# Kernel optimization log

Hardware: AMD Instinct MI355X
Metric: run time of the kernel (lower is better)

## Reference

```python
import jax, jax.numpy as jnp
import numpy as np

BATCH, N_FEATURES, D_MODEL = 8192, 8192, 1024


def setup_inputs() -> dict:
    key = jax.random.key(0)
    kx, kw = jax.random.split(key)
    # x: sparse feature activations in the original (COO); dense uniform here.
    x = jax.random.uniform(kx, (BATCH, N_FEATURES), dtype=jnp.float32)
    # Xavier-normal init for W_tr [n_features, d_model].
    std = float(np.sqrt(2.0 / (N_FEATURES + D_MODEL)))
    W_tr = jax.random.normal(kw, (N_FEATURES, D_MODEL), dtype=jnp.float32) * std
    bias = jnp.zeros((N_FEATURES,), dtype=jnp.float32)
    return {"x": x, "W_tr": W_tr, "bias": bias}


def reference(x, W_tr, bias):
    # h = x @ W_tr              : [B, n_features] @ [n_features, d_model] -> [B, d_model]
    # out = relu(h @ W_tr.T + b): [B, d_model] @ [d_model, n_features] -> [B, n_features]
    h = jnp.einsum("bf,fd->bd", x, W_tr)
    return jax.nn.relu(jnp.einsum("bd,fd->bf", h, W_tr) + bias)
```

## Files before the change

### kernel.cpp

```cpp
#include <hip/hip_runtime.h>
#include <hip/hip_bf16.h>
#include <stdint.h>

#define BATCH  8192
#define NFEAT  8192
#define DMODEL 1024

typedef unsigned short u16;
typedef __attribute__((ext_vector_type(8))) short  short8;
typedef __attribute__((ext_vector_type(4))) float  f32x4;

__device__ __forceinline__ u16 f2b(float f) {
    uint32_t u = __float_as_uint(f);
    u += 0x7fffu + ((u >> 16) & 1u);
    return (u16)(u >> 16);
}

__device__ __forceinline__ void gld16(const u16* g, void* l) {
    __builtin_amdgcn_global_load_lds(
        (const __attribute__((address_space(1))) void*)(uintptr_t)g,
        (__attribute__((address_space(3))) void*)(uint32_t)(uintptr_t)l,
        16, 0, 0);
}


__global__ void cvt_x_kernel(const float* __restrict__ x, u16* __restrict__ xb) {
    int i = blockIdx.x * blockDim.x + threadIdx.x;
    const float4* xv = (const float4*)x;
    float4 a = xv[2 * i];
    float4 b = xv[2 * i + 1];
    union { u16 u[8]; uint4 v; } o;
    o.u[0] = f2b(a.x); o.u[1] = f2b(a.y); o.u[2] = f2b(a.z); o.u[3] = f2b(a.w);
    o.u[4] = f2b(b.x); o.u[5] = f2b(b.y); o.u[6] = f2b(b.z); o.u[7] = f2b(b.w);
    ((uint4*)xb)[i] = o.v;
}

__global__ void cvt_w_kernel(const float* __restrict__ W,
                             u16* __restrict__ wb, u16* __restrict__ wt) {
    __shared__ u16 tile[64][65];
    const int f0 = blockIdx.x * 64;
    const int d0 = blockIdx.y * 64;
    const int t  = threadIdx.x;
#pragma unroll
    for (int rep = 0; rep < 16; ++rep) {
        int idx = rep * 256 + t;
        int r = idx >> 6, c = idx & 63;
        float v = W[(size_t)(f0 + r) * DMODEL + d0 + c];
        u16 u = f2b(v);
        tile[r][c] = u;
        wb[(size_t)(f0 + r) * DMODEL + d0 + c] = u;
    }
    __syncthreads();
#pragma unroll
    for (int rep = 0; rep < 16; ++rep) {
        int idx = rep * 256 + t;
        int r = idx >> 6, c = idx & 63;
        wt[(size_t)(d0 + r) * NFEAT + f0 + c] = tile[c][r];
    }
}

#define CBAR() do { asm volatile("" ::: "memory"); __builtin_amdgcn_s_barrier(); } while (0)


__global__ __launch_bounds__(512, 2)
void gemm1_relax(const u16* __restrict__ A, const u16* __restrict__ B,
                 u16* __restrict__ H, int N, int K) {
    const int NT = K >> 6;
    __shared__ __align__(1024) char lds[131072];
    const int BOFF = 98304;

    const int tid  = threadIdx.x;
    const int lane = tid & 63;
    const int wave = tid >> 6;
    const int wm   = wave >> 2;
    const int wn   = wave & 3;

    const int nwg = gridDim.x;
    const int swz = (blockIdx.x & 7) * (nwg >> 3) + (blockIdx.x >> 3);
    const int ntn = N >> 7;
    const int tm0 = (swz / ntn) << 8;
    const int tn0 = (swz % ntn) << 7;

    const int sr8 = lane >> 3;
    const int sg  = (lane & 7) ^ sr8;
    const int l15 = lane & 15, lhi = lane >> 4;
    const int ch0 = ((lhi ^ (lane & 7)) << 4);

    auto STAGE_A = [&](int tau) {
        if (tau < NT) {
            char* d = lds + (tau % 3) * 32768 + wave * 4096;
#pragma unroll
            for (int i = 0; i < 4; ++i)
                gld16(A + (size_t)(tm0 + wave * 32 + i * 8 + sr8) * K + ((size_t)tau << 6) + sg * 8,
                      d + i * 1024);
        }
    };
    auto STAGE_B = [&](int tau) {
        if (tau < NT) {
            char* d = lds + BOFF + (tau & 1) * 16384 + wave * 2048;
#pragma unroll
            for (int i = 0; i < 2; ++i)
                gld16(B + (size_t)(tn0 + wave * 16 + i * 8 + sr8) * K + ((size_t)tau << 6) + sg * 8,
                      d + i * 1024);
        }
    };

    short8 a0[4][2], a1[4][2];
    short8 b[2][2];
    f32x4  acc[8][2] = {};

    const char* Ab;
    const char* Bb;
    auto LDA0 = [&] {
#pragma unroll
        for (int fm = 0; fm < 4; ++fm) {
            a0[fm][0] = *(const short8*)(Ab + fm * 2048 + ch0);
            a0[fm][1] = *(const short8*)(Ab + fm * 2048 + (ch0 ^ 64));
        }
    };
    auto LDA1 = [&] {
#pragma unroll
        for (int fm = 0; fm < 4; ++fm) {
            a1[fm][0] = *(const short8*)(Ab + (4 + fm) * 2048 + ch0);
            a1[fm][1] = *(const short8*)(Ab + (4 + fm) * 2048 + (ch0 ^ 64));
        }
    };
    auto LDB_ = [&](int nh) {
        b[nh][0] = *(const short8*)(Bb + nh * 2048 + ch0);
        b[nh][1] = *(const short8*)(Bb + nh * 2048 + (ch0 ^ 64));
    };
    auto MMA0 = [&](int nh) {
#pragma unroll
        for (int ks = 0; ks < 2; ++ks)
#pragma unroll
            for (int fm = 0; fm < 4; ++fm)
                acc[fm][nh] = __builtin_amdgcn_mfma_f32_16x16x32_bf16(
                    a0[fm][ks], b[nh][ks], acc[fm][nh], 0, 0, 0);
    };
    auto MMA1 = [&](int nh) {
#pragma unroll
        for (int ks = 0; ks < 2; ++ks)
#pragma unroll
            for (int fm = 0; fm < 4; ++fm)
                acc[4 + fm][nh] = __builtin_amdgcn_mfma_f32_16x16x32_bf16(
                    a1[fm][ks], b[nh][ks], acc[4 + fm][nh], 0, 0, 0);
    };

    STAGE_A(0); STAGE_B(0);
    STAGE_A(1); STAGE_B(1);
    asm volatile("s_waitcnt vmcnt(6)" ::: "memory");
    __builtin_amdgcn_s_barrier();

    for (int t = 0; t < NT; ++t) {
        Ab = lds + (t % 3) * 32768 + wm * 16384 + l15 * 128;
        Bb = lds + BOFF + (t & 1) * 16384 + wn * 4096 + l15 * 128;

        LDB_(0); LDB_(1); LDA0(); LDA1();
        STAGE_A(t + 2);
        __builtin_amdgcn_s_setprio(1);
        MMA0(0); MMA0(1);
        __builtin_amdgcn_s_setprio(0);
        CBAR();
        STAGE_B(t + 2);
        __builtin_amdgcn_s_setprio(1);
        MMA1(1); MMA1(0);
        __builtin_amdgcn_s_setprio(0);
        if (t < NT - 2)       asm volatile("s_waitcnt vmcnt(6)" ::: "memory");
        else if (t == NT - 2) asm volatile("s_waitcnt vmcnt(0)" ::: "memory");
        CBAR();
    }

    u16* lu = (u16*)lds;
#pragma unroll
    for (int fm = 0; fm < 8; ++fm)
#pragma unroll
        for (int nh = 0; nh < 2; ++nh) {
            const int col  = wn * 32 + nh * 16 + l15;
            const int row0 = wm * 128 + fm * 16 + lhi * 4;
#pragma unroll
            for (int r = 0; r < 4; ++r)
                lu[(row0 + r) * 128 + col] = f2b(acc[fm][nh][r]);
        }
    __syncthreads();
    const uint4* ls = (const uint4*)lds;
#pragma unroll
    for (int s = 0; s < 8; ++s) {
        int i = s * 512 + tid;
        int row = i >> 4;
        int col = (i & 15) * 8;
        *(uint4*)(H + (size_t)(tm0 + row) * N + (tn0 + col)) = ls[i];
    }
}

__global__ __launch_bounds__(512, 2)
void gemm2_persist(const u16* __restrict__ A, const u16* __restrict__ B,
                   float* __restrict__ O, const float* __restrict__ bias,
                   int N, int K) {
    __shared__ __align__(1024) char lds[163840];
    const int BOFF = 98304;
    const int TTOT = 64;

    const int tid  = threadIdx.x;
    const int lane = tid & 63;
    const int wave = tid >> 6;
    const int wm   = wave >> 2;
    const int wn   = wave & 3;

    const int bid = blockIdx.x;
    const int xcd = bid & 7;
    const int sub = (bid >> 3) & 3;
    const int mg  = bid >> 5;
    const int tn0     = ((xcd << 2) + sub) << 8;
    const int tm_base = mg << 10;

    const int sr8 = lane >> 3;
    const int sg  = (lane & 7) ^ sr8;
    const int l15 = lane & 15, lhi = lane >> 4;
    const int ch0 = ((lhi ^ (lane & 7)) << 4);

    auto STAGE_A = [&](int tau) {
        if (tau < TTOT) {
            char* d = lds + (tau % 3) * 32768 + wave * 4096;
            const int rb = tm_base + ((tau >> 4) << 8) + wave * 32 + sr8;
            const size_t co = ((size_t)(tau & 15) << 6) + sg * 8;
#pragma unroll
            for (int i = 0; i < 4; ++i)
                gld16(A + (size_t)(rb + i * 8) * K + co, d + i * 1024);
        }
    };
    auto STAGE_B = [&](int tau) {
        if (tau < TTOT) {
            char* d = lds + BOFF + (tau & 1) * 32768 + wave * 4096;
            const int rb = tn0 + wave * 32 + sr8;
            const size_t co = ((size_t)(tau & 15) << 6) + sg * 8;
#pragma unroll
            for (int i = 0; i < 4; ++i)
                gld16(B + (size_t)(rb + i * 8) * K + co, d + i * 1024);
        }
    };

    short8 a0[4][2], a1[4][2];
    short8 b[4][2];
    f32x4  acc[8][4] = {};

    const char* Ab;
    const char* Bb;
    auto LDA0 = [&] {
#pragma unroll
        for (int fm = 0; fm < 4; ++fm) {
            a0[fm][0] = *(const short8*)(Ab + fm * 2048 + ch0);
            a0[fm][1] = *(const short8*)(Ab + fm * 2048 + (ch0 ^ 64));
        }
    };
    auto LDA1 = [&] {
#pragma unroll
        for (int fm = 0; fm < 4; ++fm) {
            a1[fm][0] = *(const short8*)(Ab + (4 + fm) * 2048 + ch0);
            a1[fm][1] = *(const short8*)(Ab + (4 + fm) * 2048 + (ch0 ^ 64));
        }
    };
    auto LDB_ = [&](int nh) {
#pragma unroll
        for (int fn = 0; fn < 2; ++fn) {
            b[nh * 2 + fn][0] = *(const short8*)(Bb + (nh * 2 + fn) * 2048 + ch0);
            b[nh * 2 + fn][1] = *(const short8*)(Bb + (nh * 2 + fn) * 2048 + (ch0 ^ 64));
        }
    };
    auto MMA0 = [&](int nh) {
#pragma unroll
        for (int ks = 0; ks < 2; ++ks)
#pragma unroll
            for (int fm = 0; fm < 4; ++fm)
#pragma unroll
                for (int fn = 0; fn < 2; ++fn)
                    acc[fm][nh * 2 + fn] = __builtin_amdgcn_mfma_f32_16x16x32_bf16(
                        a0[fm][ks], b[nh * 2 + fn][ks], acc[fm][nh * 2 + fn], 0, 0, 0);
    };
    auto MMA1 = [&](int nh) {
#pragma unroll
        for (int ks = 0; ks < 2; ++ks)
#pragma unroll
            for (int fm = 0; fm < 4; ++fm)
#pragma unroll
                for (int fn = 0; fn < 2; ++fn)
                    acc[4 + fm][nh * 2 + fn] = __builtin_amdgcn_mfma_f32_16x16x32_bf16(
                        a1[fm][ks], b[nh * 2 + fn][ks], acc[4 + fm][nh * 2 + fn], 0, 0, 0);
    };

    const int ocol = tn0 + wn * 64;
    float bv[4];
#pragma unroll
    for (int fn = 0; fn < 4; ++fn) bv[fn] = bias[ocol + fn * 16 + l15];

    STAGE_A(0); STAGE_B(0);
    STAGE_A(1); STAGE_B(1);
    asm volatile("s_waitcnt vmcnt(8)" ::: "memory");
    __builtin_amdgcn_s_barrier();

    for (int tt = 0; tt < TTOT; ++tt) {
        Ab = lds + (tt % 3) * 32768 + wm * 16384 + l15 * 128;
        Bb = lds + BOFF + (tt & 1) * 32768 + wn * 8192 + l15 * 128;

        LDB_(0); LDB_(1); LDA0(); LDA1();
        STAGE_A(tt + 2);
        __builtin_amdgcn_s_setprio(1);
        MMA0(0); MMA0(1);
        __builtin_amdgcn_s_setprio(0);
        CBAR();
        STAGE_B(tt + 2);
        __builtin_amdgcn_s_setprio(1);
        MMA1(1); MMA1(0);
        __builtin_amdgcn_s_setprio(0);
        if (tt < TTOT - 2)       asm volatile("s_waitcnt vmcnt(8)" ::: "memory");
        else if (tt == TTOT - 2) asm volatile("s_waitcnt vmcnt(0)" ::: "memory");
        CBAR();

        if ((tt & 15) == 15) {
            const int orow = tm_base + ((tt >> 4) << 8) + wm * 128;
#pragma unroll
            for (int fm = 0; fm < 8; ++fm) {
                const int row0 = orow + fm * 16 + lhi * 4;
#pragma unroll
                for (int fn = 0; fn < 4; ++fn) {
                    const int col = ocol + fn * 16 + l15;
#pragma unroll
                    for (int r = 0; r < 4; ++r) {
                        float v = acc[fm][fn][r] + bv[fn];
                        O[(size_t)(row0 + r) * N + col] = v > 0.f ? v : 0.f;
                        acc[fm][fn][r] = 0.f;
                    }
                }
            }
        }
    }
}


extern "C" void kernel_launch(void* const* d_in, const int* in_sizes, int n_in,
                              void* d_out, int out_size, void* d_ws, size_t ws_size,
                              hipStream_t stream) {
    const float* x    = (const float*)d_in[0];
    const float* W    = (const float*)d_in[1];
    const float* bias = (const float*)d_in[2];
    float* out = (float*)d_out;

    char* ws = (char*)d_ws;
    u16* xb = (u16*)ws;
    u16* wt = (u16*)(ws + 134217728);
    u16* wb = (u16*)(ws + 134217728 + 16777216);
    u16* hb = (u16*)(ws + 134217728 + 2 * 16777216);

    cvt_x_kernel<<<(BATCH * NFEAT / 8) / 256, 256, 0, stream>>>(x, xb);
    cvt_w_kernel<<<dim3(NFEAT / 64, DMODEL / 64), 256, 0, stream>>>(W, wb, wt);

    gemm1_relax<<<dim3((BATCH / 256) * (DMODEL / 128)), 512, 0, stream>>>(
        xb, wt, hb, DMODEL, NFEAT);

    gemm2_persist<<<dim3(256), 512, 0, stream>>>(
        hb, wb, out, bias, NFEAT, DMODEL);
}
```

Before: 367.2 us.

## Restructure both GEMMs into finer-grained ping-pong pipeline with per-quarter staging

Both GEMM kernels drop the triple-buffered A tile and use double buffering, which cuts LDS use (gemm1 from 128KB to 96KB, gemm2 from 160KB to 128KB). Each K-step is split into four MFMA phases, each bracketed by barriers. Global-to-LDS loads for A and B are issued in quarter/half chunks interleaved between phases, so load issue is spread across the compute instead of bunched. The tradeoffs are many more barriers per iteration and a shallower prefetch depth, which could stall if memory latency is not hidden.

```diff
diff --git a/kernel.cpp b/kernel.cpp
--- a/kernel.cpp
+++ b/kernel.cpp
@@ -59,15 +59,18 @@
     }
 }
 
-#define CBAR() do { asm volatile("" ::: "memory"); __builtin_amdgcn_s_barrier(); } while (0)
+#define SYNC_IN()  do { __builtin_amdgcn_s_barrier(); \
+                        asm volatile("s_waitcnt lgkmcnt(0)" ::: "memory"); } while (0)
+#define SYNC_OUT() do { __builtin_amdgcn_s_setprio(0); __builtin_amdgcn_s_barrier(); } while (0)
 
 
 __global__ __launch_bounds__(512, 2)
-void gemm1_relax(const u16* __restrict__ A, const u16* __restrict__ B,
-                 u16* __restrict__ H, int N, int K) {
+void gemm1_m201(const u16* __restrict__ A, const u16* __restrict__ B,
+                u16* __restrict__ H, int N, int K) {
     const int NT = K >> 6;
-    __shared__ __align__(1024) char lds[131072];
-    const int BOFF = 98304;
+    const int NIT = NT >> 1;
+    __shared__ __align__(1024) char lds[98304];
+    const int BOFF = 65536;
 
     const int tid  = threadIdx.x;
     const int lane = tid & 63;
@@ -86,22 +89,20 @@
     const int l15 = lane & 15, lhi = lane >> 4;
     const int ch0 = ((lhi ^ (lane & 7)) << 4);
 
-    auto STAGE_A = [&](int tau) {
+    auto STA = [&](int tau, int q) {
         if (tau < NT) {
-            char* d = lds + (tau % 3) * 32768 + wave * 4096;
-#pragma unroll
-            for (int i = 0; i < 4; ++i)
-                gld16(A + (size_t)(tm0 + wave * 32 + i * 8 + sr8) * K + ((size_t)tau << 6) + sg * 8,
-                      d + i * 1024);
-        }
-    };
-    auto STAGE_B = [&](int tau) {
+            const size_t co = ((size_t)tau << 6) + sg * 8;
+#pragma unroll
+            for (int j = 0; j < 2; ++j)
+                gld16(A + (size_t)(tm0 + j * 128 + q * 64 + wave * 8 + sr8) * K + co,
+                      lds + (tau & 1) * 32768 + q * 16384 + j * 8192 + wave * 1024);
+        }
+    };
+    auto STB = [&](int tau, int nh) {
         if (tau < NT) {
-            char* d = lds + BOFF + (tau & 1) * 16384 + wave * 2048;
-#pragma unroll
-            for (int i = 0; i < 2; ++i)
-                gld16(B + (size_t)(tn0 + wave * 16 + i * 8 + sr8) * K + ((size_t)tau << 6) + sg * 8,
-                      d + i * 1024);
+            const size_t co = ((size_t)tau << 6) + sg * 8;
+            gld16(B + (size_t)(tn0 + (wave >> 1) * 32 + nh * 16 + (wave & 1) * 8 + sr8) * K + co,
+                  lds + BOFF + (tau & 1) * 16384 + nh * 8192 + (wave >> 1) * 2048 + (wave & 1) * 1024);
         }
     };
 
@@ -109,25 +110,26 @@
     short8 b[2][2];
     f32x4  acc[8][2] = {};
 
-    const char* Ab;
-    const char* Bb;
-    auto LDA0 = [&] {
+    auto LDA0 = [&](int p) {
+        const char* Ab = lds + p * 32768 + wm * 8192 + l15 * 128;
 #pragma unroll
         for (int fm = 0; fm < 4; ++fm) {
             a0[fm][0] = *(const short8*)(Ab + fm * 2048 + ch0);
             a0[fm][1] = *(const short8*)(Ab + fm * 2048 + (ch0 ^ 64));
         }
     };
-    auto LDA1 = [&] {
+    auto LDA1 = [&](int p) {
+        const char* Ab = lds + p * 32768 + 16384 + wm * 8192 + l15 * 128;
 #pragma unroll
         for (int fm = 0; fm < 4; ++fm) {
-            a1[fm][0] = *(const short8*)(Ab + (4 + fm) * 2048 + ch0);
-            a1[fm][1] = *(const short8*)(Ab + (4 + fm) * 2048 + (ch0 ^ 64));
-        }
-    };
-    auto LDB_ = [&](int nh) {
-        b[nh][0] = *(const short8*)(Bb + nh * 2048 + ch0);
-        b[nh][1] = *(const short8*)(Bb + nh * 2048 + (ch0 ^ 64));
+            a1[fm][0] = *(const short8*)(Ab + fm * 2048 + ch0);
+            a1[fm][1] = *(const short8*)(Ab + fm * 2048 + (ch0 ^ 64));
+        }
+    };
+    auto LDB_ = [&](int p, int nh) {
+        const char* Bb = lds + BOFF + p * 16384 + nh * 8192 + wn * 2048 + l15 * 128;
+        b[nh][0] = *(const short8*)(Bb + ch0);
+        b[nh][1] = *(const short8*)(Bb + (ch0 ^ 64));
     };
     auto MMA0 = [&](int nh) {
 #pragma unroll
@@ -146,28 +148,68 @@
                     a1[fm][ks], b[nh][ks], acc[4 + fm][nh], 0, 0, 0);
     };
 
-    STAGE_A(0); STAGE_B(0);
-    STAGE_A(1); STAGE_B(1);
-    asm volatile("s_waitcnt vmcnt(6)" ::: "memory");
+    STA(0, 0); STB(0, 0); STA(0, 1); STB(0, 1);
+    STA(1, 0); STB(1, 0); STA(1, 1);
+    asm volatile("s_waitcnt vmcnt(5)" ::: "memory");
     __builtin_amdgcn_s_barrier();
 
-    for (int t = 0; t < NT; ++t) {
-        Ab = lds + (t % 3) * 32768 + wm * 16384 + l15 * 128;
-        Bb = lds + BOFF + (t & 1) * 16384 + wn * 4096 + l15 * 128;
-
-        LDB_(0); LDB_(1); LDA0(); LDA1();
-        STAGE_A(t + 2);
-        __builtin_amdgcn_s_setprio(1);
-        MMA0(0); MMA0(1);
+    for (int i = 0; i < NIT; ++i) {
+        const int t0 = 2 * i, t1 = 2 * i + 1;
+        const bool deep = (i < NIT - 2);
+
+        LDA0(0); LDB_(0, 0);
+        STB(t1, 1);
+        SYNC_IN();
+        __builtin_amdgcn_s_setprio(1);
+        MMA0(0);
+        SYNC_OUT();
+        LDB_(0, 1);
+        STA(t0 + 2, 0);
+        SYNC_IN();
+        __builtin_amdgcn_s_setprio(1);
+        MMA0(1);
+        SYNC_OUT();
+        LDA1(0);
+        STB(t0 + 2, 0);
+        SYNC_IN();
+        __builtin_amdgcn_s_setprio(1);
+        MMA1(1);
+        SYNC_OUT();
+        STA(t0 + 2, 1);
+        __builtin_amdgcn_s_barrier();
+        __builtin_amdgcn_s_setprio(1);
+        MMA1(0);
         __builtin_amdgcn_s_setprio(0);
-        CBAR();
-        STAGE_B(t + 2);
-        __builtin_amdgcn_s_setprio(1);
-        MMA1(1); MMA1(0);
+        if (deep) asm volatile("s_waitcnt vmcnt(5)" ::: "memory");
+        else      asm volatile("s_waitcnt vmcnt(0)" ::: "memory");
+        __builtin_amdgcn_s_barrier();
+
+        LDA0(1); LDB_(1, 0);
+        STB(t0 + 2, 1);
+        SYNC_IN();
+        __builtin_amdgcn_s_setprio(1);
+        MMA0(0);
+        SYNC_OUT();
+        LDB_(1, 1);
+        STA(t1 + 2, 0);
+        SYNC_IN();
+        __builtin_amdgcn_s_setprio(1);
+        MMA0(1);
+        SYNC_OUT();
+        LDA1(1);
+        STB(t1 + 2, 0);
+        SYNC_IN();
+        __builtin_amdgcn_s_setprio(1);
+        MMA1(1);
+        SYNC_OUT();
+        STA(t1 + 2, 1);
+        __builtin_amdgcn_s_barrier();
+        __builtin_amdgcn_s_setprio(1);
+        MMA1(0);
         __builtin_amdgcn_s_setprio(0);
-        if (t < NT - 2)       asm volatile("s_waitcnt vmcnt(6)" ::: "memory");
-        else if (t == NT - 2) asm volatile("s_waitcnt vmcnt(0)" ::: "memory");
-        CBAR();
+        if (deep) asm volatile("s_waitcnt vmcnt(5)" ::: "memory");
+        else      asm volatile("s_waitcnt vmcnt(0)" ::: "memory");
+        __builtin_amdgcn_s_barrier();
     }
 
     u16* lu = (u16*)lds;
@@ -193,12 +235,12 @@
 }
 
 __global__ __launch_bounds__(512, 2)
-void gemm2_persist(const u16* __restrict__ A, const u16* __restrict__ B,
-                   float* __restrict__ O, const float* __restrict__ bias,
-                   int N, int K) {
-    __shared__ __align__(1024) char lds[163840];
-    const int BOFF = 98304;
-    const int TTOT = 64;
+void gemm2_m201(const u16* __restrict__ A, const u16* __restrict__ B,
+                float* __restrict__ O, const float* __restrict__ bias,
+                int N, int K) {
+    const int TTOT = 64, NIT = 32;
+    __shared__ __align__(1024) char lds[131072];
+    const int BOFF = 65536;
 
     const int tid  = threadIdx.x;
     const int lane = tid & 63;
@@ -218,24 +260,25 @@
     const int l15 = lane & 15, lhi = lane >> 4;
     const int ch0 = ((lhi ^ (lane & 7)) << 4);
 
-    auto STAGE_A = [&](int tau) {
+    auto STA = [&](int tau, int q) {
         if (tau < TTOT) {
-            char* d = lds + (tau % 3) * 32768 + wave * 4096;
-            const int rb = tm_base + ((tau >> 4) << 8) + wave * 32 + sr8;
             const size_t co = ((size_t)(tau & 15) << 6) + sg * 8;
-#pragma unroll
-            for (int i = 0; i < 4; ++i)
-                gld16(A + (size_t)(rb + i * 8) * K + co, d + i * 1024);
-        }
-    };
-    auto STAGE_B = [&](int tau) {
+            const int rbase = tm_base + ((tau >> 4) << 8);
+#pragma unroll
+            for (int j = 0; j < 2; ++j)
+                gld16(A + (size_t)(rbase + j * 128 + q * 64 + wave * 8 + sr8) * K + co,
+                      lds + (tau & 1) * 32768 + q * 16384 + j * 8192 + wave * 1024);
+        }
+    };
+    auto STB = [&](int tau, int nh) {
         if (tau < TTOT) {
-            char* d = lds + BOFF + (tau & 1) * 32768 + wave * 4096;
-            const int rb = tn0 + wave * 32 + sr8;
             const size_t co = ((size_t)(tau & 15) << 6) + sg * 8;
 #pragma unroll
-            for (int i = 0; i < 4; ++i)
-                gld16(B + (size_t)(rb + i * 8) * K + co, d + i * 1024);
+            for (int j = 0; j < 2; ++j) {
+                const int cn = 2 * j + (wave >> 2);
+                gld16(B + (size_t)(tn0 + cn * 64 + nh * 32 + (wave & 3) * 8 + sr8) * K + co,
+                      lds + BOFF + (tau & 1) * 32768 + nh * 16384 + cn * 4096 + (wave & 3) * 1024);
+            }
         }
     };
 
@@ -243,27 +286,28 @@
     short8 b[4][2];
     f32x4  acc[8][4] = {};
 
-    const char* Ab;
-    const char* Bb;
-    auto LDA0 = [&] {
+    auto LDA0 = [&](int p) {
+        const char* Ab = lds + p * 32768 + wm * 8192 + l15 * 128;
 #pragma unroll
         for (int fm = 0; fm < 4; ++fm) {
             a0[fm][0] = *(const short8*)(Ab + fm * 2048 + ch0);
             a0[fm][1] = *(const short8*)(Ab + fm * 2048 + (ch0 ^ 64));
         }
     };
-    auto LDA1 = [&] {
+    auto LDA1 = [&](int p) {
+        const char* Ab = lds + p * 32768 + 16384 + wm * 8192 + l15 * 128;
 #pragma unroll
         for (int fm = 0; fm < 4; ++fm) {
-            a1[fm][0] = *(const short8*)(Ab + (4 + fm) * 2048 + ch0);
-            a1[fm][1] = *(const short8*)(Ab + (4 + fm) * 2048 + (ch0 ^ 64));
-        }
-    };
-    auto LDB_ = [&](int nh) {
+            a1[fm][0] = *(const short8*)(Ab + fm * 2048 + ch0);
+            a1[fm][1] = *(const short8*)(Ab + fm * 2048 + (ch0 ^ 64));
+        }
+    };
+    auto LDB_ = [&](int p, int nh) {
+        const char* Bb = lds + BOFF + p * 32768 + nh * 16384 + wn * 4096 + l15 * 128;
 #pragma unroll
         for (int fn = 0; fn < 2; ++fn) {
-            b[nh * 2 + fn][0] = *(const short8*)(Bb + (nh * 2 + fn) * 2048 + ch0);
-            b[nh * 2 + fn][1] = *(const short8*)(Bb + (nh * 2 + fn) * 2048 + (ch0 ^ 64));
+            b[nh * 2 + fn][0] = *(const short8*)(Bb + fn * 2048 + ch0);
+            b[nh * 2 + fn][1] = *(const short8*)(Bb + fn * 2048 + (ch0 ^ 64));
         }
     };
     auto MMA0 = [&](int nh) {
@@ -292,31 +336,73 @@
 #pragma unroll
     for (int fn = 0; fn < 4; ++fn) bv[fn] = bias[ocol + fn * 16 + l15];
 
-    STAGE_A(0); STAGE_B(0);
-    STAGE_A(1); STAGE_B(1);
-    asm volatile("s_waitcnt vmcnt(8)" ::: "memory");
+    STA(0, 0); STB(0, 0); STA(0, 1); STB(0, 1);
+    STA(1, 0); STB(1, 0); STA(1, 1);
+    asm volatile("s_waitcnt vmcnt(6)" ::: "memory");
     __builtin_amdgcn_s_barrier();
 
-    for (int tt = 0; tt < TTOT; ++tt) {
-        Ab = lds + (tt % 3) * 32768 + wm * 16384 + l15 * 128;
-        Bb = lds + BOFF + (tt & 1) * 32768 + wn * 8192 + l15 * 128;
-
-        LDB_(0); LDB_(1); LDA0(); LDA1();
-        STAGE_A(tt + 2);
-        __builtin_amdgcn_s_setprio(1);
-        MMA0(0); MMA0(1);
+    for (int i = 0; i < NIT; ++i) {
+        const int t0 = 2 * i, t1 = 2 * i + 1;
+        const bool deep = (i < NIT - 2);
+
+        LDA0(0); LDB_(0, 0);
+        STB(t1, 1);
+        asm volatile("s_waitcnt lgkmcnt(8)" ::: "memory");
+        SYNC_IN();
+        __builtin_amdgcn_s_setprio(1);
+        MMA0(0);
+        SYNC_OUT();
+        LDB_(0, 1);
+        STA(t0 + 2, 0);
+        SYNC_IN();
+        __builtin_amdgcn_s_setprio(1);
+        MMA0(1);
+        SYNC_OUT();
+        LDA1(0);
+        STB(t0 + 2, 0);
+        SYNC_IN();
+        __builtin_amdgcn_s_setprio(1);
+        MMA1(1);
+        SYNC_OUT();
+        STA(t0 + 2, 1);
+        __builtin_amdgcn_s_barrier();
+        __builtin_amdgcn_s_setprio(1);
+        MMA1(0);
         __builtin_amdgcn_s_setprio(0);
-        CBAR();
-        STAGE_B(tt + 2);
-        __builtin_amdgcn_s_setprio(1);
-        MMA1(1); MMA1(0);
+        if (deep) asm volatile("s_waitcnt vmcnt(6)" ::: "memory");
+        else      asm volatile("s_waitcnt vmcnt(0)" ::: "memory");
+        __builtin_amdgcn_s_barrier();
+
+        LDA0(1); LDB_(1, 0);
+        STB(t0 + 2, 1);
+        asm volatile("s_waitcnt lgkmcnt(8)" ::: "memory");
+        SYNC_IN();
+        __builtin_amdgcn_s_setprio(1);
+        MMA0(0);
+        SYNC_OUT();
+        LDB_(1, 1);
+        STA(t1 + 2, 0);
+        SYNC_IN();
+        __builtin_amdgcn_s_setprio(1);
+        MMA0(1);
+        SYNC_OUT();
+        LDA1(1);
+        STB(t1 + 2, 0);
+        SYNC_IN();
+        __builtin_amdgcn_s_setprio(1);
+        MMA1(1);
+        SYNC_OUT();
+        STA(t1 + 2, 1);
+        __builtin_amdgcn_s_barrier();
+        __builtin_amdgcn_s_setprio(1);
+        MMA1(0);
         __builtin_amdgcn_s_setprio(0);
-        if (tt < TTOT - 2)       asm volatile("s_waitcnt vmcnt(8)" ::: "memory");
-        else if (tt == TTOT - 2) asm volatile("s_waitcnt vmcnt(0)" ::: "memory");
-        CBAR();
-
-        if ((tt & 15) == 15) {
-            const int orow = tm_base + ((tt >> 4) << 8) + wm * 128;
+        if (deep) asm volatile("s_waitcnt vmcnt(6)" ::: "memory");
+        else      asm volatile("s_waitcnt vmcnt(0)" ::: "memory");
+        __builtin_amdgcn_s_barrier();
+
+        if ((t1 & 15) == 15) {
+            const int orow = tm_base + ((t1 >> 4) << 8) + wm * 128;
 #pragma unroll
             for (int fm = 0; fm < 8; ++fm) {
                 const int row0 = orow + fm * 16 + lhi * 4;
@@ -353,9 +439,9 @@
     cvt_x_kernel<<<(BATCH * NFEAT / 8) / 256, 256, 0, stream>>>(x, xb);
     cvt_w_kernel<<<dim3(NFEAT / 64, DMODEL / 64), 256, 0, stream>>>(W, wb, wt);
 
-    gemm1_relax<<<dim3((BATCH / 256) * (DMODEL / 128)), 512, 0, stream>>>(
+    gemm1_m201<<<dim3((BATCH / 256) * (DMODEL / 128)), 512, 0, stream>>>(
         xb, wt, hb, DMODEL, NFEAT);
 
-    gemm2_persist<<<dim3(256), 512, 0, stream>>>(
+    gemm2_m201<<<dim3(256), 512, 0, stream>>>(
         hb, wb, out, bias, NFEAT, DMODEL);
 }
```

After: 367.9 us. Within noise of the previous version (+0.2%).

## Software-pipeline LDS fragment loads across k-tiles in gemm1 with double-buffered registers

Applied to the files above, without the earlier changes.

Restructures the first GEMM's main loop so that the A-half-0 and B register fragments for the next k-tile are loaded from LDS right after the barrier, overlapping with the current tile's second MFMA half. It uses two register sets (X/Y) and a loop unrolled by two to alternate them, and cuts the barriers per iteration from two to one. The goal is to hide LDS read latency behind MFMA work. The cost is higher register pressure at two waves per SIMD, plus changed wait and barrier placement that could create buffer hazards.

```diff
diff --git a/kernel.cpp b/kernel.cpp
--- a/kernel.cpp
+++ b/kernel.cpp
@@ -63,8 +63,8 @@
 
 
 __global__ __launch_bounds__(512, 2)
-void gemm1_relax(const u16* __restrict__ A, const u16* __restrict__ B,
-                 u16* __restrict__ H, int N, int K) {
+void gemm1_pipe(const u16* __restrict__ A, const u16* __restrict__ B,
+                u16* __restrict__ H, int N, int K) {
     const int NT = K >> 6;
     __shared__ __align__(1024) char lds[131072];
     const int BOFF = 98304;
@@ -105,70 +105,83 @@
         }
     };
 
-    short8 a0[4][2], a1[4][2];
-    short8 b[2][2];
+    short8 a0X[4][2], a0Y[4][2], a1[4][2];
+    short8 bX[2][2], bY[2][2];
     f32x4  acc[8][2] = {};
 
-    const char* Ab;
-    const char* Bb;
-    auto LDA0 = [&] {
-#pragma unroll
-        for (int fm = 0; fm < 4; ++fm) {
-            a0[fm][0] = *(const short8*)(Ab + fm * 2048 + ch0);
-            a0[fm][1] = *(const short8*)(Ab + fm * 2048 + (ch0 ^ 64));
-        }
-    };
-    auto LDA1 = [&] {
-#pragma unroll
-        for (int fm = 0; fm < 4; ++fm) {
-            a1[fm][0] = *(const short8*)(Ab + (4 + fm) * 2048 + ch0);
-            a1[fm][1] = *(const short8*)(Ab + (4 + fm) * 2048 + (ch0 ^ 64));
-        }
-    };
-    auto LDB_ = [&](int nh) {
-        b[nh][0] = *(const short8*)(Bb + nh * 2048 + ch0);
-        b[nh][1] = *(const short8*)(Bb + nh * 2048 + (ch0 ^ 64));
-    };
-    auto MMA0 = [&](int nh) {
-#pragma unroll
-        for (int ks = 0; ks < 2; ++ks)
-#pragma unroll
-            for (int fm = 0; fm < 4; ++fm)
-                acc[fm][nh] = __builtin_amdgcn_mfma_f32_16x16x32_bf16(
-                    a0[fm][ks], b[nh][ks], acc[fm][nh], 0, 0, 0);
-    };
-    auto MMA1 = [&](int nh) {
-#pragma unroll
-        for (int ks = 0; ks < 2; ++ks)
-#pragma unroll
-            for (int fm = 0; fm < 4; ++fm)
-                acc[4 + fm][nh] = __builtin_amdgcn_mfma_f32_16x16x32_bf16(
-                    a1[fm][ks], b[nh][ks], acc[4 + fm][nh], 0, 0, 0);
-    };
+#define PREF(T, A0P, BP) do {                                                   \
+        if ((T) < NT) {                                                         \
+            const char* Abp = lds + ((T) % 3) * 32768 + wm * 16384 + l15 * 128; \
+            const char* Bbp = lds + BOFF + ((T) & 1) * 16384 + wn * 4096 + l15 * 128; \
+            _Pragma("unroll")                                                   \
+            for (int fm = 0; fm < 4; ++fm) {                                    \
+                A0P[fm][0] = *(const short8*)(Abp + fm * 2048 + ch0);           \
+                A0P[fm][1] = *(const short8*)(Abp + fm * 2048 + (ch0 ^ 64));    \
+            }                                                                   \
+            _Pragma("unroll")                                                   \
+            for (int nh = 0; nh < 2; ++nh) {                                    \
+                BP[nh][0] = *(const short8*)(Bbp + nh * 2048 + ch0);            \
+                BP[nh][1] = *(const short8*)(Bbp + nh * 2048 + (ch0 ^ 64));     \
+            }                                                                   \
+        }                                                                       \
+    } while (0)
+
+#define MMA0_(A0C, BC) do {                                                     \
+        _Pragma("unroll")                                                       \
+        for (int nh = 0; nh < 2; ++nh)                                          \
+            _Pragma("unroll")                                                   \
+            for (int ks = 0; ks < 2; ++ks)                                      \
+                _Pragma("unroll")                                               \
+                for (int fm = 0; fm < 4; ++fm)                                  \
+                    acc[fm][nh] = __builtin_amdgcn_mfma_f32_16x16x32_bf16(      \
+                        A0C[fm][ks], BC[nh][ks], acc[fm][nh], 0, 0, 0);         \
+    } while (0)
+
+#define MMA1_(BC) do {                                                          \
+        _Pragma("unroll")                                                       \
+        for (int nh = 0; nh < 2; ++nh)                                          \
+            _Pragma("unroll")                                                   \
+            for (int ks = 0; ks < 2; ++ks)                                      \
+                _Pragma("unroll")                                               \
+                for (int fm = 0; fm < 4; ++fm)                                  \
+                    acc[4 + fm][nh] = __builtin_amdgcn_mfma_f32_16x16x32_bf16(  \
+                        a1[fm][ks], BC[nh][ks], acc[4 + fm][nh], 0, 0, 0);      \
+    } while (0)
+
+#define GTILE(T, A0C, BC, A0P, BP) do {                                         \
+                  \
+        const char* Ab_ = lds + ((T) % 3) * 32768 + wm * 16384 + l15 * 128;     \
+        _Pragma("unroll")                                                       \
+        for (int fm = 0; fm < 4; ++fm) {                                        \
+            a1[fm][0] = *(const short8*)(Ab_ + (4 + fm) * 2048 + ch0);          \
+            a1[fm][1] = *(const short8*)(Ab_ + (4 + fm) * 2048 + (ch0 ^ 64));   \
+        }                                                                       \
+        STAGE_A((T) + 2);                                                       \
+        __builtin_amdgcn_s_setprio(1);                                          \
+        MMA0_(A0C, BC);                                                         \
+        __builtin_amdgcn_s_setprio(0);                                          \
+        STAGE_B((T) + 2);                                                       \
+                    \
+        if ((T) < NT - 2) asm volatile("s_waitcnt vmcnt(6)" ::: "memory");      \
+        else              asm volatile("s_waitcnt vmcnt(0)" ::: "memory");      \
+        CBAR();             \
+        PREF((T) + 1, A0P, BP);                                                 \
+        __builtin_amdgcn_s_setprio(1);                                          \
+        MMA1_(BC);                                                              \
+        __builtin_amdgcn_s_setprio(0);                                          \
+    } while (0)
 
     STAGE_A(0); STAGE_B(0);
     STAGE_A(1); STAGE_B(1);
     asm volatile("s_waitcnt vmcnt(6)" ::: "memory");
     __builtin_amdgcn_s_barrier();
-
-    for (int t = 0; t < NT; ++t) {
-        Ab = lds + (t % 3) * 32768 + wm * 16384 + l15 * 128;
-        Bb = lds + BOFF + (t & 1) * 16384 + wn * 4096 + l15 * 128;
-
-        LDB_(0); LDB_(1); LDA0(); LDA1();
-        STAGE_A(t + 2);
-        __builtin_amdgcn_s_setprio(1);
-        MMA0(0); MMA0(1);
-        __builtin_amdgcn_s_setprio(0);
-        CBAR();
-        STAGE_B(t + 2);
-        __builtin_amdgcn_s_setprio(1);
-        MMA1(1); MMA1(0);
-        __builtin_amdgcn_s_setprio(0);
-        if (t < NT - 2)       asm volatile("s_waitcnt vmcnt(6)" ::: "memory");
-        else if (t == NT - 2) asm volatile("s_waitcnt vmcnt(0)" ::: "memory");
-        CBAR();
-    }
+    PREF(0, a0X, bX);
+
+    for (int t = 0; t < NT; t += 2) {
+        GTILE(t,     a0X, bX, a0Y, bY);
+        GTILE(t + 1, a0Y, bY, a0X, bX);
+    }
+    __syncthreads();
 
     u16* lu = (u16*)lds;
 #pragma unroll
@@ -190,6 +203,10 @@
         int col = (i & 15) * 8;
         *(uint4*)(H + (size_t)(tm0 + row) * N + (tn0 + col)) = ls[i];
     }
+#undef GTILE
+#undef PREF
+#undef MMA0_
+#undef MMA1_
 }
 
 __global__ __launch_bounds__(512, 2)
@@ -353,7 +370,7 @@
     cvt_x_kernel<<<(BATCH * NFEAT / 8) / 256, 256, 0, stream>>>(x, xb);
     cvt_w_kernel<<<dim3(NFEAT / 64, DMODEL / 64), 256, 0, stream>>>(W, wb, wt);
 
-    gemm1_relax<<<dim3((BATCH / 256) * (DMODEL / 128)), 512, 0, stream>>>(
+    gemm1_pipe<<<dim3((BATCH / 256) * (DMODEL / 128)), 512, 0, stream>>>(
         xb, wt, hb, DMODEL, NFEAT);
 
     gemm2_persist<<<dim3(256), 512, 0, stream>>>(
```

After: 345.7 us. 1.06x faster.
